# Kernel tuning notes

Measured on AMD Instinct MI355X. Metric: run time of the kernel, lower is better.

## Reference

```python
import jax, jax.numpy as jnp
import numpy as np

C, P, PQ, D, B, HW = 32, 64, 4, 2048, 256, 7
N = HW * HW  # 49 spatial positions


def _bn(x, g, b):
    # eval-mode BatchNorm2d with running_mean=0, running_var=1
    s = g / jnp.sqrt(1.0 + 1e-5)
    return x * s[None, :, None, None] + b[None, :, None, None]


def _g1x1(x, w):
    # grouped 1x1 conv: x [B, C*pin, H, W], w [C, pout, pin]
    Bs, _, Hh, Ww = x.shape
    xg = x.reshape(Bs, C, w.shape[2], Hh, Ww)
    y = jnp.einsum('bcihw,coi->bcohw', xg, w)
    return y.reshape(Bs, C * w.shape[1], Hh, Ww)


def setup_inputs() -> dict:
    key = jax.random.key(0)
    ks = iter(jax.random.split(key, 40))
    def rn(shape, s=1.0):
        return jax.random.normal(next(ks), shape, jnp.float32) * s
    inp = {
        'x': rn((B, D, HW, HW)),
        'W1': rn((C * P, D), 0.02), 'g1': 1.0 + rn((C * P,), 0.1), 'b1': rn((C * P,), 0.1),
        'W2': rn((C * P, P, 3, 3), 0.04), 'g2': 1.0 + rn((C * P,), 0.1), 'b2': rn((C * P,), 0.1),
        'Wq': rn((C, PQ, P), 0.1), 'gq': 1.0 + rn((C * PQ,), 0.1), 'bq': rn((C * PQ,), 0.1),
        'Wk': rn((C, PQ, P), 0.1), 'gk': 1.0 + rn((C * PQ,), 0.1), 'bk': rn((C * PQ,), 0.1),
        'Wout': rn((C, PQ, P), 0.1), 'gout': 1.0 + rn((C * PQ,), 0.1), 'bout': rn((C * PQ,), 0.1),
        'Wcr': rn((C, C, PQ), 0.1), 'gcr': 1.0 + rn((C * C,), 0.1), 'bcr': rn((C * C,), 0.1),
        'gcr1': 1.0 + rn((C * PQ,), 0.1), 'bcr1': rn((C * PQ,), 0.1),
        'Wa': rn((C, P, PQ), 0.1), 'ba': rn((C * P,), 0.1),
        'Wb': rn((C, P, PQ), 0.1), 'bb': rn((C * P,), 0.1),
        'W3': rn((D, C * P), 0.02), 'g3': 1.0 + rn((D,), 0.1), 'b3': rn((D,), 0.1),
    }
    return inp


def reference(x, W1, g1, b1, W2, g2, b2, Wq, gq, bq, Wk, gk, bk,
              Wout, gout, bout, Wcr, gcr, bcr, gcr1, bcr1,
              Wa, ba, Wb, bb, W3, g3, b3):
    # stem: 1x1 conv + BN, grouped 3x3 conv + BN
    Xc = _bn(jnp.einsum('bdhw,ed->behw', x, W1), g1, b1)             # [B,2048,7,7]
    Zc = _bn(jax.lax.conv_general_dilated(
        Xc, W2, (1, 1), 'SAME', feature_group_count=C,
        dimension_numbers=('NCHW', 'OIHW', 'NCHW')), g2, b2)         # [B,2048,7,7]

    # channel self-attention: per-group q(1xp_) @ k(p_xN)
    pooled = jnp.mean(Zc, axis=(2, 3), keepdims=True)                # AvgPool2d(7) -> 1x1
    q = _bn(_g1x1(pooled, Wq), gq, bq).reshape(-1, C, PQ)            # [B,c,p_]
    k = _bn(_g1x1(Zc, Wk), gk, bk).reshape(-1, C, PQ, N)             # [B,c,p_,N]
    scores = jnp.einsum('bcp,bcpn->bcn', q, k)                       # [B,c,N]
    # torch Softmax2d on 3D [B,1,N] normalizes dim -3 == batch dim (faithful quirk)
    M = jax.nn.softmax(scores, axis=0)                               # [B,c,N]

    Zg = Zc.reshape(-1, C, P, N)
    zout = jnp.einsum('bcpn,bcn->bcp', Zg, M).reshape(-1, C * P, 1, 1)
    hc = _bn(_g1x1(zout, Wout), gout, bout)                          # [B,128,1,1]

    # channel-relation: A [B,c,c] mixes H [B,c,p_]
    A = jnp.tanh(_bn(_g1x1(hc, Wcr), gcr, bcr)).reshape(-1, C, C)
    A = jnp.swapaxes(A, 1, 2)                                        # chunk/cat transpose
    Hm = hc.reshape(-1, C, PQ)                                       # [B,c,p_]
    mix = jnp.matmul(A, Hm) + Hm                                     # [B,c,p_]
    hc_ = jax.nn.relu(_bn(mix.reshape(-1, C * PQ, 1, 1), gcr1, bcr1)).reshape(-1, C, PQ)

    # broadcast back to spatial via attention maps
    M_ = M / jnp.max(M)
    Mchc = jnp.einsum('bcp,bcn->bcpn', hc_, M_).reshape(-1, C * PQ, HW, HW)

    alpha = _g1x1(Mchc, Wa) + ba[None, :, None, None]                # [B,2048,7,7]
    beta = _g1x1(Mchc, Wb) + bb[None, :, None, None]
    Xc_ = jax.nn.relu(Zc * alpha + beta)
    cm = Zc * Xc_

    OUT = _bn(jnp.einsum('behw,de->bdhw', cm, W3), g3, b3)
    return OUT + x
```

## Files before the change

### kernel.cpp

```cpp
#include <hip/hip_runtime.h>
#include <hip/hip_bf16.h>
#include <stdint.h>

#define DI __device__ __forceinline__

typedef __attribute__((ext_vector_type(8))) short short8;
typedef __attribute__((ext_vector_type(4))) float floatx4;

DI float bf2f(short u) {
  union { unsigned int i; float f; } v;
  v.i = ((unsigned int)(unsigned short)u) << 16;
  return v.f;
}
DI short f2bf(float f) {
  union { float f; unsigned int i; } v; v.f = f;
  unsigned int r = v.i + 0x7FFFu + ((v.i >> 16) & 1u);
  return (short)(r >> 16);
}

DI void gload16(const void* g, void* l) {
  __builtin_amdgcn_global_load_lds(
      (const __attribute__((address_space(1))) void*)g,
      (__attribute__((address_space(3))) void*)l,
      16, 0, 0);
}

__global__ __launch_bounds__(256) void k_cvt(const float* __restrict__ src,
                                             short* __restrict__ dst, int n) {
  int i = blockIdx.x * 256 + threadIdx.x;
  if (i < n) dst[i] = f2bf(src[i]);
}

__global__ __launch_bounds__(256) void k_w2r(const float* __restrict__ W2,
                                             short* __restrict__ W2R) {
  int idx = blockIdx.x * 256 + threadIdx.x;
  if (idx >= 32 * 9 * 64 * 64) return;
  int pi = idx & 63;
  int po = (idx >> 6) & 63;
  int ct = idx >> 12;
  int tap = ct % 9, c = ct / 9;
  W2R[idx] = f2bf(W2[((c * 64 + po) * 64 + pi) * 9 + tap]);
}

__global__ __launch_bounds__(256) void k_xt(const float* __restrict__ x,
                                            short* __restrict__ xT) {
  __shared__ float tile[64 * 49];
  int b = blockIdx.x, dc = blockIdx.y;
  const float* xp = x + ((size_t)b * 2048 + dc * 64) * 49;
  for (int i = threadIdx.x; i < 64 * 49; i += 256) tile[i] = xp[i];
  __syncthreads();
  for (int i = threadIdx.x; i < 64 * 49; i += 256) {
    int n = i >> 6, dl = i & 63;
    xT[((size_t)(b * 49 + n)) * 2048 + dc * 64 + dl] = f2bf(tile[dl * 49 + n]);
  }
}

__global__ __launch_bounds__(512, 4) void k_gemm1(
    const short* __restrict__ xT, const short* __restrict__ W1b,
    const float* __restrict__ g1, const float* __restrict__ b1,
    short* __restrict__ XcPad) {
  __shared__ __attribute__((aligned(16))) short As[2][8192];
  __shared__ __attribute__((aligned(16))) short Bs[2][8192];
  const int tid = threadIdx.x;
  const int wave = tid >> 6, lane = tid & 63;
  const int wg = blockIdx.x;
  const int swz = (wg & 7) * 196 + (wg >> 3);
  const int mt = swz >> 4, et = swz & 15;
  const int r8 = tid >> 3, p0 = tid & 7;
  const int gsw = ((p0 ^ (r8 & 7)) << 3);
  const short* aR0 = xT + (size_t)(mt * 128 + r8) * 2048 + gsw;
  const short* aR1 = aR0 + (size_t)64 * 2048;
  const short* bR0 = W1b + (size_t)(et * 128 + r8) * 2048 + gsw;
  const short* bR1 = bR0 + (size_t)64 * 2048;
  const int lo0 = r8 * 64 + p0 * 8;
  const int lo1 = (r8 + 64) * 64 + p0 * 8;
  const int wr = wave >> 2, wc = wave & 3;
  const int la = lane & 15, q = lane >> 4, l7 = lane & 7;
  const int cx0 = ((q) ^ l7) << 3;
  const int cx1 = ((4 + q) ^ l7) << 3;
  int arow[4], brow[2];
#pragma unroll
  for (int i = 0; i < 4; ++i) arow[i] = (wr * 64 + i * 16 + la) * 64;
#pragma unroll
  for (int j = 0; j < 2; ++j) brow[j] = (wc * 32 + j * 16 + la) * 64;
  floatx4 acc[4][2] = {};
  auto STAGE = [&](int buf, int kt) {
    const int ko = kt * 64;
    gload16(aR0 + ko, &As[buf][lo0]);
    gload16(aR1 + ko, &As[buf][lo1]);
    gload16(bR0 + ko, &Bs[buf][lo0]);
    gload16(bR1 + ko, &Bs[buf][lo1]);
  };
  auto COMPUTE = [&](int buf) {
#pragma unroll
    for (int kk = 0; kk < 2; ++kk) {
      const int cx = kk ? cx1 : cx0;
      short8 a[4], b[2];
#pragma unroll
      for (int i = 0; i < 4; ++i) a[i] = *(const short8*)&As[buf][arow[i] + cx];
#pragma unroll
      for (int j = 0; j < 2; ++j) b[j] = *(const short8*)&Bs[buf][brow[j] + cx];
#pragma unroll
      for (int i = 0; i < 4; ++i)
#pragma unroll
        for (int j = 0; j < 2; ++j)
          acc[i][j] = __builtin_amdgcn_mfma_f32_16x16x32_bf16(a[i], b[j], acc[i][j], 0, 0, 0);
    }
  };
  STAGE(0, 0);
  int cur = 0;
#pragma unroll 1
  for (int kt = 0; kt < 31; ++kt) {
    STAGE(cur ^ 1, kt + 1);
    asm volatile("s_waitcnt vmcnt(4)" ::: "memory");
    __builtin_amdgcn_s_barrier();
    COMPUTE(cur);
    __builtin_amdgcn_s_barrier();
    cur ^= 1;
  }
  asm volatile("s_waitcnt vmcnt(0)" ::: "memory");
  __builtin_amdgcn_s_barrier();
  COMPUTE(cur);
  const float rs = rsqrtf(1.0f + 1e-5f);
  size_t abase[16];
#pragma unroll
  for (int i = 0; i < 4; ++i)
#pragma unroll
    for (int r = 0; r < 4; ++r) {
      int m = mt * 128 + wr * 64 + i * 16 + (lane >> 4) * 4 + r;
      int bb = m / 49, n = m % 49, h = n / 7, w = n % 7;
      abase[i * 4 + r] = ((size_t)bb * 81 + (h + 1) * 9 + (w + 1)) * 2048;
    }
#pragma unroll
  for (int j = 0; j < 2; ++j) {
    int e = et * 128 + wc * 32 + j * 16 + (lane & 15);
    float s = g1[e] * rs, bo = b1[e];
#pragma unroll
    for (int i = 0; i < 4; ++i)
#pragma unroll
      for (int r = 0; r < 4; ++r)
        XcPad[abase[i * 4 + r] + e] = f2bf(acc[i][j][r] * s + bo);
  }
}

__global__ __launch_bounds__(512, 4) void k_conv(
    const short* __restrict__ XcPad, const short* __restrict__ W2R,
    const float* __restrict__ g2, const float* __restrict__ b2,
    short* __restrict__ ZcT) {
  __shared__ __attribute__((aligned(16))) short As[2][8192];
  __shared__ __attribute__((aligned(16))) short Ws[2][4096];
  const int tid = threadIdx.x;
  const int wave = tid >> 6, lane = tid & 63;
  const int wg = blockIdx.x;
  const int swz = (wg & 7) * 392 + (wg >> 3);
  const int mt = swz >> 5, c = swz & 31;
  const int r8 = tid >> 3, p0 = tid & 7;
  const int gsw = ((p0 ^ (r8 & 7)) << 3);
  int m0 = mt * 128 + r8;
  int b0 = m0 / 49, n0 = m0 % 49, h0 = n0 / 7, w0 = n0 % 7;
  int m1 = m0 + 64;
  int b1v = m1 / 49, n1 = m1 % 49, h1 = n1 / 7, w1 = n1 % 7;
  const short* aB0 = XcPad + ((size_t)b0 * 81 + (h0 + 1) * 9 + (w0 + 1)) * 2048 + c * 64 + gsw;
  const short* aB1 = XcPad + ((size_t)b1v * 81 + (h1 + 1) * 9 + (w1 + 1)) * 2048 + c * 64 + gsw;
  const short* wB = W2R + (size_t)c * 9 * 4096 + r8 * 64 + gsw;
  const int lo0 = r8 * 64 + p0 * 8;
  const int lo1 = (r8 + 64) * 64 + p0 * 8;
  const int wr = wave >> 1, wc = wave & 1;
  const int la = lane & 15, q = lane >> 4, l7 = lane & 7;
  const int cx0 = ((q) ^ l7) << 3;
  const int cx1 = ((4 + q) ^ l7) << 3;
  int arow[2], brow[2];
#pragma unroll
  for (int i = 0; i < 2; ++i) arow[i] = (wr * 32 + i * 16 + la) * 64;
#pragma unroll
  for (int j = 0; j < 2; ++j) brow[j] = (wc * 32 + j * 16 + la) * 64;
  floatx4 acc[2][2] = {};
  auto STAGE = [&](int buf, int tap) {
    const int toff = ((tap / 3 - 1) * 9 + (tap % 3 - 1)) * 2048;
    gload16(aB0 + toff, &As[buf][lo0]);
    gload16(aB1 + toff, &As[buf][lo1]);
    gload16(wB + tap * 4096, &Ws[buf][lo0]);
  };
  auto COMPUTE = [&](int buf) {
#pragma unroll
    for (int kk = 0; kk < 2; ++kk) {
      const int cx = kk ? cx1 : cx0;
      short8 a[2], b[2];
#pragma unroll
      for (int i = 0; i < 2; ++i) a[i] = *(const short8*)&As[buf][arow[i] + cx];
#pragma unroll
      for (int j = 0; j < 2; ++j) b[j] = *(const short8*)&Ws[buf][brow[j] + cx];
#pragma unroll
      for (int i = 0; i < 2; ++i)
#pragma unroll
        for (int j = 0; j < 2; ++j)
          acc[i][j] = __builtin_amdgcn_mfma_f32_16x16x32_bf16(a[i], b[j], acc[i][j], 0, 0, 0);
    }
  };
  STAGE(0, 0);
  int cur = 0;
#pragma unroll 1
  for (int tap = 0; tap < 8; ++tap) {
    STAGE(cur ^ 1, tap + 1);
    asm volatile("s_waitcnt vmcnt(3)" ::: "memory");
    __builtin_amdgcn_s_barrier();
    COMPUTE(cur);
    __builtin_amdgcn_s_barrier();
    cur ^= 1;
  }
  asm volatile("s_waitcnt vmcnt(0)" ::: "memory");
  __builtin_amdgcn_s_barrier();
  COMPUTE(cur);
  const float rs = rsqrtf(1.0f + 1e-5f);
#pragma unroll
  for (int j = 0; j < 2; ++j) {
    int e = c * 64 + wc * 32 + j * 16 + (lane & 15);
    float s = g2[e] * rs, bo = b2[e];
#pragma unroll
    for (int i = 0; i < 2; ++i)
#pragma unroll
      for (int r = 0; r < 4; ++r) {
        int m = mt * 128 + wr * 32 + i * 16 + (lane >> 4) * 4 + r;
        ZcT[(size_t)m * 2048 + e] = f2bf(acc[i][j][r] * s + bo);
      }
  }
}

__global__ __launch_bounds__(256) void k_scores(
    const short* __restrict__ ZcT, const float* __restrict__ Wq,
    const float* __restrict__ gq, const float* __restrict__ bq,
    const float* __restrict__ Wk, const float* __restrict__ gk,
    const float* __restrict__ bk, float* __restrict__ scores) {
  int b = blockIdx.x, t = threadIdx.x;
  __shared__ float pooled[2048];
  __shared__ float qv[128];
  const float rs = rsqrtf(1.0f + 1e-5f);
  for (int e = t; e < 2048; e += 256) {
    float s = 0.f;
    for (int n = 0; n < 49; ++n) s += bf2f(ZcT[((size_t)(b * 49 + n)) * 2048 + e]);
    pooled[e] = s * (1.0f / 49.0f);
  }
  __syncthreads();
  if (t < 128) {
    int c = t >> 2;
    float s = 0.f;
    for (int pi = 0; pi < 64; ++pi) s += Wq[t * 64 + pi] * pooled[c * 64 + pi];
    qv[t] = s * gq[t] * rs + bq[t];
  }
  __syncthreads();
  for (int idx = t; idx < 1568; idx += 256) {
    int c = idx / 49, n = idx % 49;
    const short8* z = (const short8*)&ZcT[((size_t)(b * 49 + n)) * 2048 + c * 64];
    float acc[4] = {0.f, 0.f, 0.f, 0.f};
#pragma unroll
    for (int p8 = 0; p8 < 8; ++p8) {
      short8 v = z[p8];
#pragma unroll
      for (int j = 0; j < 8; ++j) {
        float zv = bf2f(v[j]);
#pragma unroll
        for (int pq = 0; pq < 4; ++pq)
          acc[pq] += Wk[(c * 4 + pq) * 64 + p8 * 8 + j] * zv;
      }
    }
    float sc = 0.f;
#pragma unroll
    for (int pq = 0; pq < 4; ++pq) {
      float kv = acc[pq] * gk[c * 4 + pq] * rs + bk[c * 4 + pq];
      sc += qv[c * 4 + pq] * kv;
    }
    scores[b * 1568 + idx] = sc;
  }
}

__global__ __launch_bounds__(256) void k_softmax(const float* __restrict__ scores,
                                                 float* __restrict__ Msm,
                                                 unsigned int* __restrict__ maxM) {
  int cn = blockIdx.x, t = threadIdx.x;
  float v = scores[t * 1568 + cn];
  __shared__ float red[4], red2[4];
  float m = v;
#pragma unroll
  for (int o = 1; o < 64; o <<= 1) m = fmaxf(m, __shfl_xor(m, o));
  if ((t & 63) == 0) red[t >> 6] = m;
  __syncthreads();
  m = fmaxf(fmaxf(red[0], red[1]), fmaxf(red[2], red[3]));
  float e = expf(v - m);
  float s = e;
#pragma unroll
  for (int o = 1; o < 64; o <<= 1) s += __shfl_xor(s, o);
  if ((t & 63) == 0) red2[t >> 6] = s;
  __syncthreads();
  s = red2[0] + red2[1] + red2[2] + red2[3];
  Msm[t * 1568 + cn] = e / s;
  if (t == 0) atomicMax(maxM, __float_as_uint(1.0f / s));
}

__global__ __launch_bounds__(256) void k_tail(
    const short* __restrict__ ZcT, const float* __restrict__ Msm,
    const float* __restrict__ Wout, const float* __restrict__ gout,
    const float* __restrict__ bout, const float* __restrict__ Wcr,
    const float* __restrict__ gcr, const float* __restrict__ bcr,
    const float* __restrict__ gcr1, const float* __restrict__ bcr1,
    const float* __restrict__ Wa, const float* __restrict__ Wb,
    float* __restrict__ va, float* __restrict__ vb) {
  int b = blockIdx.x, t = threadIdx.x;
  __shared__ float Mrow[1568];
  __shared__ float zout[2048];
  __shared__ float hcl[128];
  __shared__ float tb[1024];
  __shared__ float hcp[128];
  const float rs = rsqrtf(1.0f + 1e-5f);
  for (int i = t; i < 1568; i += 256) Mrow[i] = Msm[b * 1568 + i];
  __syncthreads();
  for (int e = t; e < 2048; e += 256) {
    int c = e >> 6;
    float s = 0.f;
    for (int n = 0; n < 49; ++n)
      s += bf2f(ZcT[((size_t)(b * 49 + n)) * 2048 + e]) * Mrow[c * 49 + n];
    zout[e] = s;
  }
  __syncthreads();
  if (t < 128) {
    int c = t >> 2;
    float s = 0.f;
    for (int p = 0; p < 64; ++p) s += Wout[t * 64 + p] * zout[c * 64 + p];
    hcl[t] = s * gout[t] * rs + bout[t];
  }
  __syncthreads();
  for (int i = t; i < 1024; i += 256) {
    int c = i >> 5;
    float s = 0.f;
#pragma unroll
    for (int k = 0; k < 4; ++k) s += Wcr[i * 4 + k] * hcl[c * 4 + k];
    tb[i] = tanhf(s * gcr[i] * rs + bcr[i]);
  }
  __syncthreads();
  if (t < 128) {
    int i = t >> 2, pq = t & 3;
    float s = hcl[t];
    for (int j = 0; j < 32; ++j) s += tb[j * 32 + i] * hcl[j * 4 + pq];
    hcp[t] = fmaxf(s * gcr1[t] * rs + bcr1[t], 0.0f);
  }
  __syncthreads();
  for (int e = t; e < 2048; e += 256) {
    int c = e >> 6;
    float sa = 0.f, sb = 0.f;
#pragma unroll
    for (int pq = 0; pq < 4; ++pq) {
      float h = hcp[c * 4 + pq];
      sa += Wa[e * 4 + pq] * h;
      sb += Wb[e * 4 + pq] * h;
    }
    va[b * 2048 + e] = sa;
    vb[b * 2048 + e] = sb;
  }
}

__global__ __launch_bounds__(256) void k_cm(
    const short* __restrict__ ZcT, const float* __restrict__ Msm,
    const unsigned int* __restrict__ maxM, const float* __restrict__ va,
    const float* __restrict__ vb, const float* __restrict__ ba,
    const float* __restrict__ bb, short* __restrict__ cm) {
  int m = blockIdx.x;
  int b = m / 49, n = m % 49;
  __shared__ float Minv[32];
  if (threadIdx.x < 32) {
    float mx = __uint_as_float(*maxM);
    Minv[threadIdx.x] = Msm[b * 1568 + threadIdx.x * 49 + n] / mx;
  }
  __syncthreads();
  const int e0 = threadIdx.x * 8;
  short8 z8 = *(const short8*)&ZcT[(size_t)m * 2048 + e0];
  const float mi = Minv[e0 >> 6];
  short8 o;
#pragma unroll
  for (int j = 0; j < 8; ++j) {
    float zc = bf2f(z8[j]);
    float al = va[b * 2048 + e0 + j] * mi + ba[e0 + j];
    float bt = vb[b * 2048 + e0 + j] * mi + bb[e0 + j];
    float xc = fmaxf(zc * al + bt, 0.0f);
    o[j] = f2bf(zc * xc);
  }
  *(short8*)&cm[(size_t)m * 2048 + e0] = o;
}

__global__ __launch_bounds__(512, 4) void k_gemm2(
    const short* __restrict__ W3b, const short* __restrict__ cm,
    const float* __restrict__ g3, const float* __restrict__ b3,
    const float* __restrict__ x, float* __restrict__ out) {
  __shared__ __attribute__((aligned(16))) short As[2][8192];
  __shared__ __attribute__((aligned(16))) short Bs[2][8192];
  const int tid = threadIdx.x;
  const int wave = tid >> 6, lane = tid & 63;
  const int wg = blockIdx.x;
  const int swz = (wg & 7) * 196 + (wg >> 3);
  const int mt = swz >> 4, dt = swz & 15;
  const int r8 = tid >> 3, p0 = tid & 7;
  const int gsw = ((p0 ^ (r8 & 7)) << 3);
  const short* aR0 = W3b + (size_t)(dt * 128 + r8) * 2048 + gsw;
  const short* aR1 = aR0 + (size_t)64 * 2048;
  const short* bR0 = cm + (size_t)(mt * 128 + r8) * 2048 + gsw;
  const short* bR1 = bR0 + (size_t)64 * 2048;
  const int lo0 = r8 * 64 + p0 * 8;
  const int lo1 = (r8 + 64) * 64 + p0 * 8;
  const int wr = wave >> 2, wc = wave & 3;
  const int la = lane & 15, q = lane >> 4, l7 = lane & 7;
  const int cx0 = ((q) ^ l7) << 3;
  const int cx1 = ((4 + q) ^ l7) << 3;
  int arow[4], brow[2];
#pragma unroll
  for (int i = 0; i < 4; ++i) arow[i] = (wr * 64 + i * 16 + la) * 64;
#pragma unroll
  for (int j = 0; j < 2; ++j) brow[j] = (wc * 32 + j * 16 + la) * 64;
  floatx4 acc[4][2] = {};
  auto STAGE = [&](int buf, int kt) {
    const int ko = kt * 64;
    gload16(aR0 + ko, &As[buf][lo0]);
    gload16(aR1 + ko, &As[buf][lo1]);
    gload16(bR0 + ko, &Bs[buf][lo0]);
    gload16(bR1 + ko, &Bs[buf][lo1]);
  };
  auto COMPUTE = [&](int buf) {
#pragma unroll
    for (int kk = 0; kk < 2; ++kk) {
      const int cx = kk ? cx1 : cx0;
      short8 a[4], b[2];
#pragma unroll
      for (int i = 0; i < 4; ++i) a[i] = *(const short8*)&As[buf][arow[i] + cx];
#pragma unroll
      for (int j = 0; j < 2; ++j) b[j] = *(const short8*)&Bs[buf][brow[j] + cx];
#pragma unroll
      for (int i = 0; i < 4; ++i)
#pragma unroll
        for (int j = 0; j < 2; ++j)
          acc[i][j] = __builtin_amdgcn_mfma_f32_16x16x32_bf16(a[i], b[j], acc[i][j], 0, 0, 0);
    }
  };
  STAGE(0, 0);
  int cur = 0;
#pragma unroll 1
  for (int kt = 0; kt < 31; ++kt) {
    STAGE(cur ^ 1, kt + 1);
    asm volatile("s_waitcnt vmcnt(4)" ::: "memory");
    __builtin_amdgcn_s_barrier();
    COMPUTE(cur);
    __builtin_amdgcn_s_barrier();
    cur ^= 1;
  }
  asm volatile("s_waitcnt vmcnt(0)" ::: "memory");
  __builtin_amdgcn_s_barrier();
  COMPUTE(cur);
  const float rs = rsqrtf(1.0f + 1e-5f);
  size_t cbb[2];
#pragma unroll
  for (int j = 0; j < 2; ++j) {
    int m = mt * 128 + wc * 32 + j * 16 + (lane & 15);
    int bb = m / 49, n = m % 49;
    cbb[j] = (size_t)bb * (2048 * 49) + n;
  }
#pragma unroll
  for (int i = 0; i < 4; ++i)
#pragma unroll
    for (int r = 0; r < 4; ++r) {
      int d = dt * 128 + wr * 64 + i * 16 + (lane >> 4) * 4 + r;
      float s = g3[d] * rs, bo = b3[d];
      size_t dterm = (size_t)d * 49;
#pragma unroll
      for (int j = 0; j < 2; ++j) {
        size_t adr = cbb[j] + dterm;
        out[adr] = acc[i][j][r] * s + bo + x[adr];
      }
    }
}

extern "C" void kernel_launch(void* const* d_in, const int* in_sizes, int n_in,
                              void* d_out, int out_size, void* d_ws, size_t ws_size,
                              hipStream_t stream) {
  (void)in_sizes; (void)n_in; (void)out_size; (void)ws_size;
  const float* x    = (const float*)d_in[0];
  const float* W1   = (const float*)d_in[1];
  const float* g1   = (const float*)d_in[2];
  const float* b1   = (const float*)d_in[3];
  const float* W2   = (const float*)d_in[4];
  const float* g2   = (const float*)d_in[5];
  const float* b2   = (const float*)d_in[6];
  const float* Wq   = (const float*)d_in[7];
  const float* gq   = (const float*)d_in[8];
  const float* bq   = (const float*)d_in[9];
  const float* Wk   = (const float*)d_in[10];
  const float* gk   = (const float*)d_in[11];
  const float* bk   = (const float*)d_in[12];
  const float* Wout = (const float*)d_in[13];
  const float* gout = (const float*)d_in[14];
  const float* bout = (const float*)d_in[15];
  const float* Wcr  = (const float*)d_in[16];
  const float* gcr  = (const float*)d_in[17];
  const float* bcr  = (const float*)d_in[18];
  const float* gcr1 = (const float*)d_in[19];
  const float* bcr1 = (const float*)d_in[20];
  const float* Wa   = (const float*)d_in[21];
  const float* ba   = (const float*)d_in[22];
  const float* Wb   = (const float*)d_in[23];
  const float* bb   = (const float*)d_in[24];
  const float* W3   = (const float*)d_in[25];
  const float* g3   = (const float*)d_in[26];
  const float* b3   = (const float*)d_in[27];
  float* out = (float*)d_out;

  char* ws = (char*)d_ws;
  short* XcPad  = (short*)(ws + 0);
  short* xT     = (short*)(ws + 84934656);
  short* ZcT    = (short*)(ws + 136314880);
  short* W1b    = (short*)(ws + 187695104);
  short* W3b    = (short*)(ws + 196083712);
  short* W2R    = (short*)(ws + 204472320);
  float* scores = (float*)(ws + 209059840);
  float* Msm    = (float*)(ws + 210665472);
  float* va     = (float*)(ws + 212271104);
  float* vb     = (float*)(ws + 214368256);
  unsigned int* maxM = (unsigned int*)(ws + 216465408);
  short* cm = xT;

  hipMemsetAsync(XcPad, 0, 84934656, stream);
  hipMemsetAsync(maxM, 0, 4, stream);

  k_cvt<<<16384, 256, 0, stream>>>(W1, W1b, 4194304);
  k_cvt<<<16384, 256, 0, stream>>>(W3, W3b, 4194304);
  k_w2r<<<4608, 256, 0, stream>>>(W2, W2R);
  k_xt<<<dim3(256, 32), 256, 0, stream>>>(x, xT);
  k_gemm1<<<1568, 512, 0, stream>>>(xT, W1b, g1, b1, XcPad);
  k_conv<<<3136, 512, 0, stream>>>(XcPad, W2R, g2, b2, ZcT);
  k_scores<<<256, 256, 0, stream>>>(ZcT, Wq, gq, bq, Wk, gk, bk, scores);
  k_softmax<<<1568, 256, 0, stream>>>(scores, Msm, maxM);
  k_tail<<<256, 256, 0, stream>>>(ZcT, Msm, Wout, gout, bout, Wcr, gcr, bcr,
                                  gcr1, bcr1, Wa, Wb, va, vb);
  k_cm<<<12544, 256, 0, stream>>>(ZcT, Msm, maxM, va, vb, ba, bb, cm);
  k_gemm2<<<1568, 512, 0, stream>>>(W3b, cm, g3, b3, x, out);
}
```

Measured before the change: 850.7 us.

## Deepen GEMM and conv LDS pipelines and vectorize pooling reductions

Both 1x1 GEMMs now use a 4-stage LDS ring with K-tiles of 32 in place of a 2-stage ring with K-tiles of 64. The grouped conv moves to a 3-stage ring. All three kernels raise wave priority around the MFMA block with s_setprio. This is meant to keep more global loads in flight and hide memory latency. The pooling and attention-weighted reductions are also rewritten to load 8 bf16 values per thread with vector loads. The cost is more barriers per K step, and the hand-tuned waitcnt and buffer-index logic must stay correct.

Result: no change. 858.2 us (+0.9%).

```diff
diff --git a/kernel.cpp b/kernel.cpp
--- a/kernel.cpp
+++ b/kernel.cpp
@@ -59,68 +59,66 @@
     const short* __restrict__ xT, const short* __restrict__ W1b,
     const float* __restrict__ g1, const float* __restrict__ b1,
     short* __restrict__ XcPad) {
-  __shared__ __attribute__((aligned(16))) short As[2][8192];
-  __shared__ __attribute__((aligned(16))) short Bs[2][8192];
+  __shared__ __attribute__((aligned(16))) short As[4][4096];
+  __shared__ __attribute__((aligned(16))) short Bs[4][4096];
   const int tid = threadIdx.x;
   const int wave = tid >> 6, lane = tid & 63;
   const int wg = blockIdx.x;
   const int swz = (wg & 7) * 196 + (wg >> 3);
   const int mt = swz >> 4, et = swz & 15;
-  const int r8 = tid >> 3, p0 = tid & 7;
-  const int gsw = ((p0 ^ (r8 & 7)) << 3);
-  const short* aR0 = xT + (size_t)(mt * 128 + r8) * 2048 + gsw;
-  const short* aR1 = aR0 + (size_t)64 * 2048;
-  const short* bR0 = W1b + (size_t)(et * 128 + r8) * 2048 + gsw;
-  const short* bR1 = bR0 + (size_t)64 * 2048;
-  const int lo0 = r8 * 64 + p0 * 8;
-  const int lo1 = (r8 + 64) * 64 + p0 * 8;
+  const int r4 = tid >> 2, p0 = tid & 3;
+  const int gsw = ((p0 ^ (r4 & 3)) << 3);
+  const short* aR = xT + (size_t)(mt * 128 + r4) * 2048 + gsw;
+  const short* bR = W1b + (size_t)(et * 128 + r4) * 2048 + gsw;
+  const int lo = tid * 8;
   const int wr = wave >> 2, wc = wave & 3;
-  const int la = lane & 15, q = lane >> 4, l7 = lane & 7;
-  const int cx0 = ((q) ^ l7) << 3;
-  const int cx1 = ((4 + q) ^ l7) << 3;
+  const int la = lane & 15, q = lane >> 4;
+  const int cx = ((q ^ (la & 3)) << 3);
   int arow[4], brow[2];
 #pragma unroll
-  for (int i = 0; i < 4; ++i) arow[i] = (wr * 64 + i * 16 + la) * 64;
-#pragma unroll
-  for (int j = 0; j < 2; ++j) brow[j] = (wc * 32 + j * 16 + la) * 64;
+  for (int i = 0; i < 4; ++i) arow[i] = (wr * 64 + i * 16 + la) * 32;
+#pragma unroll
+  for (int j = 0; j < 2; ++j) brow[j] = (wc * 32 + j * 16 + la) * 32;
   floatx4 acc[4][2] = {};
   auto STAGE = [&](int buf, int kt) {
-    const int ko = kt * 64;
-    gload16(aR0 + ko, &As[buf][lo0]);
-    gload16(aR1 + ko, &As[buf][lo1]);
-    gload16(bR0 + ko, &Bs[buf][lo0]);
-    gload16(bR1 + ko, &Bs[buf][lo1]);
+    const int ko = kt * 32;
+    gload16(aR + ko, &As[buf][lo]);
+    gload16(bR + ko, &Bs[buf][lo]);
   };
   auto COMPUTE = [&](int buf) {
-#pragma unroll
-    for (int kk = 0; kk < 2; ++kk) {
-      const int cx = kk ? cx1 : cx0;
-      short8 a[4], b[2];
-#pragma unroll
-      for (int i = 0; i < 4; ++i) a[i] = *(const short8*)&As[buf][arow[i] + cx];
-#pragma unroll
-      for (int j = 0; j < 2; ++j) b[j] = *(const short8*)&Bs[buf][brow[j] + cx];
-#pragma unroll
-      for (int i = 0; i < 4; ++i)
-#pragma unroll
-        for (int j = 0; j < 2; ++j)
-          acc[i][j] = __builtin_amdgcn_mfma_f32_16x16x32_bf16(a[i], b[j], acc[i][j], 0, 0, 0);
-    }
+    short8 a[4], b[2];
+#pragma unroll
+    for (int i = 0; i < 4; ++i) a[i] = *(const short8*)&As[buf][arow[i] + cx];
+#pragma unroll
+    for (int j = 0; j < 2; ++j) b[j] = *(const short8*)&Bs[buf][brow[j] + cx];
+#pragma unroll
+    for (int i = 0; i < 4; ++i)
+#pragma unroll
+      for (int j = 0; j < 2; ++j)
+        acc[i][j] = __builtin_amdgcn_mfma_f32_16x16x32_bf16(a[i], b[j], acc[i][j], 0, 0, 0);
   };
   STAGE(0, 0);
-  int cur = 0;
+  STAGE(1, 1);
+  STAGE(2, 2);
 #pragma unroll 1
-  for (int kt = 0; kt < 31; ++kt) {
-    STAGE(cur ^ 1, kt + 1);
-    asm volatile("s_waitcnt vmcnt(4)" ::: "memory");
+  for (int t = 0; t < 61; ++t) {
+    STAGE((t + 3) & 3, t + 3);
+    asm volatile("s_waitcnt vmcnt(6)" ::: "memory");
     __builtin_amdgcn_s_barrier();
-    COMPUTE(cur);
+    __builtin_amdgcn_s_setprio(1);
+    COMPUTE(t & 3);
+    __builtin_amdgcn_s_setprio(0);
     __builtin_amdgcn_s_barrier();
-    cur ^= 1;
-  }
+  }
+  asm volatile("s_waitcnt vmcnt(4)" ::: "memory");
+  __builtin_amdgcn_s_barrier();
+  COMPUTE(1);
+  asm volatile("s_waitcnt vmcnt(2)" ::: "memory");
+  __builtin_amdgcn_s_barrier();
+  COMPUTE(2);
   asm volatile("s_waitcnt vmcnt(0)" ::: "memory");
   __builtin_amdgcn_s_barrier();
-  COMPUTE(cur);
+  COMPUTE(3);
   const float rs = rsqrtf(1.0f + 1e-5f);
   size_t abase[16];
 #pragma unroll
@@ -147,8 +145,8 @@
     const short* __restrict__ XcPad, const short* __restrict__ W2R,
     const float* __restrict__ g2, const float* __restrict__ b2,
     short* __restrict__ ZcT) {
-  __shared__ __attribute__((aligned(16))) short As[2][8192];
-  __shared__ __attribute__((aligned(16))) short Ws[2][4096];
+  __shared__ __attribute__((aligned(16))) short As[3][8192];
+  __shared__ __attribute__((aligned(16))) short Ws[3][4096];
   const int tid = threadIdx.x;
   const int wave = tid >> 6, lane = tid & 63;
   const int wg = blockIdx.x;
@@ -163,8 +161,8 @@
   const short* aB0 = XcPad + ((size_t)b0 * 81 + (h0 + 1) * 9 + (w0 + 1)) * 2048 + c * 64 + gsw;
   const short* aB1 = XcPad + ((size_t)b1v * 81 + (h1 + 1) * 9 + (w1 + 1)) * 2048 + c * 64 + gsw;
   const short* wB = W2R + (size_t)c * 9 * 4096 + r8 * 64 + gsw;
-  const int lo0 = r8 * 64 + p0 * 8;
-  const int lo1 = (r8 + 64) * 64 + p0 * 8;
+  const int lo0 = tid * 8;
+  const int lo1 = lo0 + 4096;
   const int wr = wave >> 1, wc = wave & 1;
   const int la = lane & 15, q = lane >> 4, l7 = lane & 7;
   const int cx0 = ((q) ^ l7) << 3;
@@ -198,19 +196,26 @@
     }
   };
   STAGE(0, 0);
-  int cur = 0;
+  STAGE(1, 1);
+  int sb = 2, cb = 0;
 #pragma unroll 1
-  for (int tap = 0; tap < 8; ++tap) {
-    STAGE(cur ^ 1, tap + 1);
-    asm volatile("s_waitcnt vmcnt(3)" ::: "memory");
+  for (int t = 0; t < 7; ++t) {
+    STAGE(sb, t + 2);
+    sb = (sb == 2) ? 0 : sb + 1;
+    asm volatile("s_waitcnt vmcnt(6)" ::: "memory");
     __builtin_amdgcn_s_barrier();
-    COMPUTE(cur);
+    __builtin_amdgcn_s_setprio(1);
+    COMPUTE(cb);
+    __builtin_amdgcn_s_setprio(0);
+    cb = (cb == 2) ? 0 : cb + 1;
     __builtin_amdgcn_s_barrier();
-    cur ^= 1;
-  }
+  }
+  asm volatile("s_waitcnt vmcnt(3)" ::: "memory");
+  __builtin_amdgcn_s_barrier();
+  COMPUTE(1);
   asm volatile("s_waitcnt vmcnt(0)" ::: "memory");
   __builtin_amdgcn_s_barrier();
-  COMPUTE(cur);
+  COMPUTE(2);
   const float rs = rsqrtf(1.0f + 1e-5f);
 #pragma unroll
   for (int j = 0; j < 2; ++j) {
@@ -235,10 +240,16 @@
   __shared__ float pooled[2048];
   __shared__ float qv[128];
   const float rs = rsqrtf(1.0f + 1e-5f);
-  for (int e = t; e < 2048; e += 256) {
-    float s = 0.f;
-    for (int n = 0; n < 49; ++n) s += bf2f(ZcT[((size_t)(b * 49 + n)) * 2048 + e]);
-    pooled[e] = s * (1.0f / 49.0f);
+  {
+    const int e0 = t * 8;
+    float pool[8] = {};
+    for (int n = 0; n < 49; ++n) {
+      short8 v = *(const short8*)&ZcT[((size_t)(b * 49 + n)) * 2048 + e0];
+#pragma unroll
+      for (int j = 0; j < 8; ++j) pool[j] += bf2f(v[j]);
+    }
+#pragma unroll
+    for (int j = 0; j < 8; ++j) pooled[e0 + j] = pool[j] * (1.0f / 49.0f);
   }
   __syncthreads();
   if (t < 128) {
@@ -313,12 +324,17 @@
   const float rs = rsqrtf(1.0f + 1e-5f);
   for (int i = t; i < 1568; i += 256) Mrow[i] = Msm[b * 1568 + i];
   __syncthreads();
-  for (int e = t; e < 2048; e += 256) {
-    int c = e >> 6;
-    float s = 0.f;
-    for (int n = 0; n < 49; ++n)
-      s += bf2f(ZcT[((size_t)(b * 49 + n)) * 2048 + e]) * Mrow[c * 49 + n];
-    zout[e] = s;
+  {
+    const int e0 = t * 8, c = t >> 3;
+    float zo[8] = {};
+    for (int n = 0; n < 49; ++n) {
+      short8 v = *(const short8*)&ZcT[((size_t)(b * 49 + n)) * 2048 + e0];
+      float mw = Mrow[c * 49 + n];
+#pragma unroll
+      for (int j = 0; j < 8; ++j) zo[j] += bf2f(v[j]) * mw;
+    }
+#pragma unroll
+    for (int j = 0; j < 8; ++j) zout[e0 + j] = zo[j];
   }
   __syncthreads();
   if (t < 128) {
@@ -389,68 +405,66 @@
     const short* __restrict__ W3b, const short* __restrict__ cm,
     const float* __restrict__ g3, const float* __restrict__ b3,
     const float* __restrict__ x, float* __restrict__ out) {
-  __shared__ __attribute__((aligned(16))) short As[2][8192];
-  __shared__ __attribute__((aligned(16))) short Bs[2][8192];
+  __shared__ __attribute__((aligned(16))) short As[4][4096];
+  __shared__ __attribute__((aligned(16))) short Bs[4][4096];
   const int tid = threadIdx.x;
   const int wave = tid >> 6, lane = tid & 63;
   const int wg = blockIdx.x;
   const int swz = (wg & 7) * 196 + (wg >> 3);
   const int mt = swz >> 4, dt = swz & 15;
-  const int r8 = tid >> 3, p0 = tid & 7;
-  const int gsw = ((p0 ^ (r8 & 7)) << 3);
-  const short* aR0 = W3b + (size_t)(dt * 128 + r8) * 2048 + gsw;
-  const short* aR1 = aR0 + (size_t)64 * 2048;
-  const short* bR0 = cm + (size_t)(mt * 128 + r8) * 2048 + gsw;
-  const short* bR1 = bR0 + (size_t)64 * 2048;
-  const int lo0 = r8 * 64 + p0 * 8;
-  const int lo1 = (r8 + 64) * 64 + p0 * 8;
+  const int r4 = tid >> 2, p0 = tid & 3;
+  const int gsw = ((p0 ^ (r4 & 3)) << 3);
+  const short* aR = W3b + (size_t)(dt * 128 + r4) * 2048 + gsw;
+  const short* bR = cm + (size_t)(mt * 128 + r4) * 2048 + gsw;
+  const int lo = tid * 8;
   const int wr = wave >> 2, wc = wave & 3;
-  const int la = lane & 15, q = lane >> 4, l7 = lane & 7;
-  const int cx0 = ((q) ^ l7) << 3;
-  const int cx1 = ((4 + q) ^ l7) << 3;
+  const int la = lane & 15, q = lane >> 4;
+  const int cx = ((q ^ (la & 3)) << 3);
   int arow[4], brow[2];
 #pragma unroll
-  for (int i = 0; i < 4; ++i) arow[i] = (wr * 64 + i * 16 + la) * 64;
-#pragma unroll
-  for (int j = 0; j < 2; ++j) brow[j] = (wc * 32 + j * 16 + la) * 64;
+  for (int i = 0; i < 4; ++i) arow[i] = (wr * 64 + i * 16 + la) * 32;
+#pragma unroll
+  for (int j = 0; j < 2; ++j) brow[j] = (wc * 32 + j * 16 + la) * 32;
   floatx4 acc[4][2] = {};
   auto STAGE = [&](int buf, int kt) {
-    const int ko = kt * 64;
-    gload16(aR0 + ko, &As[buf][lo0]);
-    gload16(aR1 + ko, &As[buf][lo1]);
-    gload16(bR0 + ko, &Bs[buf][lo0]);
-    gload16(bR1 + ko, &Bs[buf][lo1]);
+    const int ko = kt * 32;
+    gload16(aR + ko, &As[buf][lo]);
+    gload16(bR + ko, &Bs[buf][lo]);
   };
   auto COMPUTE = [&](int buf) {
-#pragma unroll
-    for (int kk = 0; kk < 2; ++kk) {
-      const int cx = kk ? cx1 : cx0;
-      short8 a[4], b[2];
-#pragma unroll
-      for (int i = 0; i < 4; ++i) a[i] = *(const short8*)&As[buf][arow[i] + cx];
-#pragma unroll
-      for (int j = 0; j < 2; ++j) b[j] = *(const short8*)&Bs[buf][brow[j] + cx];
-#pragma unroll
-      for (int i = 0; i < 4; ++i)
-#pragma unroll
-        for (int j = 0; j < 2; ++j)
-          acc[i][j] = __builtin_amdgcn_mfma_f32_16x16x32_bf16(a[i], b[j], acc[i][j], 0, 0, 0);
-    }
+    short8 a[4], b[2];
+#pragma unroll
+    for (int i = 0; i < 4; ++i) a[i] = *(const short8*)&As[buf][arow[i] + cx];
+#pragma unroll
+    for (int j = 0; j < 2; ++j) b[j] = *(const short8*)&Bs[buf][brow[j] + cx];
+#pragma unroll
+    for (int i = 0; i < 4; ++i)
+#pragma unroll
+      for (int j = 0; j < 2; ++j)
+        acc[i][j] = __builtin_amdgcn_mfma_f32_16x16x32_bf16(a[i], b[j], acc[i][j], 0, 0, 0);
   };
   STAGE(0, 0);
-  int cur = 0;
+  STAGE(1, 1);
+  STAGE(2, 2);
 #pragma unroll 1
-  for (int kt = 0; kt < 31; ++kt) {
-    STAGE(cur ^ 1, kt + 1);
-    asm volatile("s_waitcnt vmcnt(4)" ::: "memory");
+  for (int t = 0; t < 61; ++t) {
+    STAGE((t + 3) & 3, t + 3);
+    asm volatile("s_waitcnt vmcnt(6)" ::: "memory");
     __builtin_amdgcn_s_barrier();
-    COMPUTE(cur);
+    __builtin_amdgcn_s_setprio(1);
+    COMPUTE(t & 3);
+    __builtin_amdgcn_s_setprio(0);
     __builtin_amdgcn_s_barrier();
-    cur ^= 1;
-  }
+  }
+  asm volatile("s_waitcnt vmcnt(4)" ::: "memory");
+  __builtin_amdgcn_s_barrier();
+  COMPUTE(1);
+  asm volatile("s_waitcnt vmcnt(2)" ::: "memory");
+  __builtin_amdgcn_s_barrier();
+  COMPUTE(2);
   asm volatile("s_waitcnt vmcnt(0)" ::: "memory");
   __builtin_amdgcn_s_barrier();
-  COMPUTE(cur);
+  COMPUTE(3);
   const float rs = rsqrtf(1.0f + 1e-5f);
   size_t cbb[2];
 #pragma unroll
```
